# Performance work log

Hardware: AMD Instinct MI355X
Metric: run time of the kernel (lower is better)

The kernel has to match this reference:

```python
import jax, jax.numpy as jnp
import numpy as np

S, IN, M, V, K = 8192, 512, 512, 50, 8


def setup_inputs() -> dict:
    key = jax.random.key(0)
    ks = jax.random.split(key, 6)
    sc = 0.02
    inp = {
        "inputs": jax.random.normal(ks[0], (S, IN), jnp.float32),
        "Wioux": sc * jax.random.normal(ks[1], (5 * M, IN), jnp.float32),
        "bioux": jnp.zeros((5 * M,), jnp.float32),
        "Wiouh": sc * jax.random.normal(ks[2], (5 * M, M), jnp.float32),
        "biouh": jnp.zeros((5 * M,), jnp.float32),
        "Wlx": sc * jax.random.normal(ks[3], (M, IN), jnp.float32),
        "blx": jnp.zeros((M,), jnp.float32),
        "Wlh": sc * jax.random.normal(ks[4], (M, M), jnp.float32),
        "blh": jnp.zeros((M,), jnp.float32),
        "lb": jnp.ones((V, M), jnp.float32),  # nn.Parameter(torch.ones(V, M))
    }
    rng = np.random.default_rng(0)
    t = np.arange(S)[:, None]
    u1 = rng.random((S, K)); u2 = rng.random((S, K))
    rel_fw = (u1 * np.maximum(t, 1)).astype(np.int32)                     # idx < t
    rel_bw = np.minimum(t + 1 + (u2 * np.maximum(S - 1 - t, 1)).astype(np.int64), S - 1).astype(np.int32)  # idx > t
    mask_fw = rng.random((S, K)) < 0.6
    mask_fw[0, :] = False      # t=0 fwd has no relatives in the original
    mask_bw = rng.random((S, K)) < 0.6
    mask_bw[S - 1, :] = False  # t=S-1 bwd has no relatives
    inp["rel_fw"] = jnp.asarray(rel_fw)
    inp["dep_fw"] = jnp.asarray(rng.integers(0, V, (S, K)).astype(np.int32))
    inp["mask_fw"] = jnp.asarray(mask_fw)
    inp["rel_bw"] = jnp.asarray(rel_bw)
    inp["dep_bw"] = jnp.asarray(rng.integers(0, V, (S, K)).astype(np.int32))
    inp["mask_bw"] = jnp.asarray(mask_bw)
    return inp


def _syn_lstm(inputs, Wioux, bioux, Wiouh, biouh, Wlx, blx, Wlh, blh, lb,
              rel, dep, mask, order):
    """One direction; order gives the timestep visit order. Returns [S, M]."""
    mdim = Wlh.shape[0]

    def step(carry, t):
        Hbuf, h_prev, c_prev = carry
        x = inputs[t]
        ious = Wioux @ x + bioux + Wiouh @ h_prev + biouh          # [5M]
        c0, c1, c2, c3, c4 = jnp.split(ious, 5)
        # NOTE: original torch code assigns (i,o,f,s,u)=(sig(i),sig(o),sig(s),sig(f),tanh(u)),
        # i.e. gate f uses chunk 3 and gate s uses chunk 2 -- reproduced faithfully.
        i = jax.nn.sigmoid(c0)
        o = jax.nn.sigmoid(c1)
        f = jax.nn.sigmoid(c3)
        s = jax.nn.sigmoid(c2)
        u = jnp.tanh(c4)
        c = f * c_prev + i * u
        h = o * jnp.tanh(c)
        rel_h = Hbuf[rel[t]]                                       # [K, M] gather of prior hiddens
        l = jax.nn.sigmoid(rel_h @ Wlh.T + blh + (Wlx @ x + blx) + lb[dep[t]])  # [K, M]
        agg = jnp.sum(l * rel_h * mask[t][:, None].astype(rel_h.dtype), axis=0)  # [M]
        h = h + s * jnp.tanh(agg)   # if all masked: agg=0, tanh(0)=0 -> empty-relative branch
        Hbuf = Hbuf.at[t].set(h)
        return (Hbuf, h, c), None

    Hbuf0 = jnp.zeros((inputs.shape[0], mdim), inputs.dtype)
    z = jnp.zeros((mdim,), inputs.dtype)
    (Hbuf, _, _), _ = jax.lax.scan(step, (Hbuf0, z, z), order)
    return Hbuf


def reference(inputs, Wioux, bioux, Wiouh, biouh, Wlx, blx, Wlh, blh, lb,
              rel_fw, dep_fw, mask_fw, rel_bw, dep_bw, mask_bw):
    n = inputs.shape[0]
    Hfw = _syn_lstm(inputs, Wioux, bioux, Wiouh, biouh, Wlx, blx, Wlh, blh, lb,
                    rel_fw, dep_fw, mask_fw, jnp.arange(n))
    Hbw = _syn_lstm(inputs, Wioux, bioux, Wiouh, biouh, Wlx, blx, Wlh, blh, lb,
                    rel_bw, dep_bw, mask_bw, jnp.arange(n - 1, -1, -1))
    return jnp.concatenate([Hfw, Hbw], axis=1)   # [S, 2*M]
```

## Files before the change

kernel.cpp:

```cpp
#include <hip/hip_runtime.h>

#define S_LEN 8192
#define KREL 8
#define WPD 128

typedef float f4 __attribute__((ext_vector_type(4)));
typedef unsigned long long u64;

__device__ __forceinline__ float sigmf(float x) { return 1.0f / (1.0f + __expf(-x)); }
__device__ __forceinline__ float tanhfast(float x) { return 1.0f - 2.0f / (__expf(2.0f * x) + 1.0f); }

__global__ void k_maskcvt(const unsigned char* __restrict__ src,
                          unsigned char* __restrict__ dst, int n)
{
  const unsigned int* w = (const unsigned int*)src;
  __shared__ int s_i32, s_f32;
  if (threadIdx.x == 0) { s_i32 = 1; s_f32 = 1; }
  __syncthreads();
  int i32ok = 1, f32ok = 1;
  for (int i = threadIdx.x; i < 1024; i += blockDim.x) {
    const unsigned int v = w[i];
    if (v != 0u && v != 1u) i32ok = 0;
    if (v != 0u && v != 0x3F800000u) f32ok = 0;
  }
  if (!i32ok) atomicAnd(&s_i32, 0);
  if (!f32ok) atomicAnd(&s_f32, 0);
  __syncthreads();
  const int wide = (s_i32 || s_f32);
  for (int i = blockIdx.x * blockDim.x + threadIdx.x; i < n; i += gridDim.x * blockDim.x)
    dst[i] = wide ? (w[i] ? 1 : 0) : (src[i] ? 1 : 0);
}

__global__ __launch_bounds__(256)
void k_gemm(const float* __restrict__ X, const float* __restrict__ Wioux,
            const float* __restrict__ Wlx, const float* __restrict__ bioux,
            const float* __restrict__ biouh, const float* __restrict__ blx,
            const float* __restrict__ blh, float* __restrict__ P)
{
  __shared__ float As[16][64];
  __shared__ float Bs[16][64];
  const int t0 = blockIdx.x * 64;
  const int r0 = blockIdx.y * 64;
  const int tid = threadIdx.x;
  const int tx = tid & 15, ty = tid >> 4;
  const int si = tid >> 2, sk = (tid & 3) << 2;
  const int rB = r0 + si;
  const float* brow = (rB < 2560) ? (Wioux + (size_t)rB * 512)
                                  : (Wlx + (size_t)(rB - 2560) * 512);
  const float* arow = X + (size_t)(t0 + si) * 512;
  float acc[4][4] = {};
  for (int k0 = 0; k0 < 512; k0 += 16) {
    const float4 av = *(const float4*)(arow + k0 + sk);
    const float4 bv = *(const float4*)(brow + k0 + sk);
    __syncthreads();
    As[sk + 0][si] = av.x; As[sk + 1][si] = av.y; As[sk + 2][si] = av.z; As[sk + 3][si] = av.w;
    Bs[sk + 0][si] = bv.x; Bs[sk + 1][si] = bv.y; Bs[sk + 2][si] = bv.z; Bs[sk + 3][si] = bv.w;
    __syncthreads();
#pragma unroll
    for (int kk = 0; kk < 16; ++kk) {
      const float4 a = *(const float4*)&As[kk][ty * 4];
      const float4 b = *(const float4*)&Bs[kk][tx * 4];
      acc[0][0] += a.x * b.x; acc[0][1] += a.x * b.y; acc[0][2] += a.x * b.z; acc[0][3] += a.x * b.w;
      acc[1][0] += a.y * b.x; acc[1][1] += a.y * b.y; acc[1][2] += a.y * b.z; acc[1][3] += a.y * b.w;
      acc[2][0] += a.z * b.x; acc[2][1] += a.z * b.y; acc[2][2] += a.z * b.z; acc[2][3] += a.z * b.w;
      acc[3][0] += a.w * b.x; acc[3][1] += a.w * b.y; acc[3][2] += a.w * b.z; acc[3][3] += a.w * b.w;
    }
  }
#pragma unroll
  for (int i = 0; i < 4; ++i) {
    const int t = t0 + ty * 4 + i;
#pragma unroll
    for (int j = 0; j < 4; ++j) {
      const int r = r0 + tx * 4 + j;
      const float bias = (r < 2560) ? (bioux[r] + biouh[r]) : (blx[r - 2560] + blh[r - 2560]);
      P[(size_t)t * 3072 + r] = acc[i][j] + bias;
    }
  }
}

__global__ __launch_bounds__(256, 1)
void k_rec(const float* __restrict__ Wiouh, const float* __restrict__ Wlh,
           const float* __restrict__ P, const float* __restrict__ lb,
           const int* __restrict__ rel_fw, const int* __restrict__ dep_fw,
           const unsigned char* __restrict__ mask_fw,
           const int* __restrict__ rel_bw, const int* __restrict__ dep_bw,
           const unsigned char* __restrict__ mask_bw,
           float* __restrict__ Gfw, float* __restrict__ Gbw,
           u64* rec, float* __restrict__ out)
{
  __shared__ float wlds[4 * 6 * 512];
  __shared__ float hs[2][512];
  const int wg  = blockIdx.x;
  const int dir = wg / WPD;
  const int w   = wg % WPD;
  const int tid = threadIdx.x;
  const int grp = tid >> 6;
  const int lane = tid & 63;
  const int kl = lane & 7;
  const int m = w * 4 + grp;
  const int dircol = dir * 512;
  const int* rel = dir ? rel_bw : rel_fw;
  const int* dep = dir ? dep_bw : dep_fw;
  const unsigned char* msk = dir ? mask_bw : mask_fw;
  float* Gbuf = dir ? Gbw : Gfw;

  {
    const float* rows[6];
#pragma unroll
    for (int rg = 0; rg < 5; ++rg) rows[rg] = Wiouh + (size_t)(rg * 512 + m) * 512;
    rows[5] = Wlh + (size_t)m * 512;
#pragma unroll
    for (int rg = 0; rg < 6; ++rg)
#pragma unroll
      for (int q = 0; q < 2; ++q)
        *(f4*)&wlds[(size_t)grp * 3072 + rg * 512 + q * 256 + lane * 4] =
            *(const f4*)(rows[rg] + q * 256 + lane * 4);
  }
  const unsigned wbase = (unsigned)(uintptr_t)&wlds[(size_t)grp * 3072 + lane * 4];

  hs[0][tid] = 0.0f; hs[0][tid + 256] = 0.0f;

  float cstate = 0.0f, hprev = 0.0f, gprev = 0.0f;

  int jjU, mkU, jjN, mkN, depN;
  float Hg, Gg, LBg;
  float p0, p1, p2, p3, p4, p5;
  {
    const int t0 = dir ? (S_LEN - 1) : 0;
    const int t1 = dir ? (S_LEN - 2) : 1;
    jjU = rel[t0 * KREL + kl]; mkU = (int)msk[t0 * KREL + kl];
    Hg  = out[(size_t)jjU * 1024 + dircol + m];
    Gg  = Gbuf[(size_t)jjU * 512 + m];
    LBg = lb[(size_t)dep[t0 * KREL + kl] * 512 + m];
    const float* prow = P + (size_t)t0 * 3072;
    p0 = prow[m];        p1 = prow[512 + m];  p2 = prow[1024 + m];
    p3 = prow[1536 + m]; p4 = prow[2048 + m]; p5 = prow[2560 + m];
    jjN = rel[t1 * KREL + kl]; mkN = (int)msk[t1 * KREL + kl]; depN = dep[t1 * KREL + kl];
  }
  __syncthreads();

#pragma unroll 1
  for (int s = 0; s < S_LEN; ++s) {
    const int t = dir ? (S_LEN - 1 - s) : s;
    const int tn = dir ? (t - 1) : (t + 1);
    const int prevt  = dir ? (t + 1) : (t - 1);
    const int prevt2 = dir ? (t + 2) : (t - 2);

    f4 wf[6][2];
#pragma unroll
    for (int rg = 0; rg < 6; ++rg)
#pragma unroll
      for (int q = 0; q < 2; ++q)
        asm volatile("ds_read_b128 %0, %1 offset:%2"
                     : "=v"(wf[rg][q])
                     : "v"(wbase), "i"((rg * 512 + q * 256) * 4)
                     : "memory");

    if (s > 0) {
      const int pb = (((s - 1) & 1) * 2 + dir) * 512;
      u64 v0 = __hip_atomic_load(rec + pb + tid,       __ATOMIC_RELAXED, __HIP_MEMORY_SCOPE_AGENT);
      u64 v1 = __hip_atomic_load(rec + pb + tid + 256, __ATOMIC_RELAXED, __HIP_MEMORY_SCOPE_AGENT);
      for (;;) {
        const bool ok0 = (unsigned)(v0 >> 32) >= (unsigned)s;
        const bool ok1 = (unsigned)(v1 >> 32) >= (unsigned)s;
        if (ok0 && ok1) break;
        if (!ok0) v0 = __hip_atomic_load(rec + pb + tid,       __ATOMIC_RELAXED, __HIP_MEMORY_SCOPE_AGENT);
        if (!ok1) v1 = __hip_atomic_load(rec + pb + tid + 256, __ATOMIC_RELAXED, __HIP_MEMORY_SCOPE_AGENT);
      }
      hs[s & 1][tid]       = __uint_as_float((unsigned)v0);
      hs[s & 1][tid + 256] = __uint_as_float((unsigned)v1);
      __syncthreads();
    }

    asm volatile("s_waitcnt lgkmcnt(0)" ::: "memory");
    float4 h4[2];
#pragma unroll
    for (int q = 0; q < 2; ++q) h4[q] = *(const float4*)&hs[s & 1][lane * 4 + 256 * q];
    float dsum[6];
#pragma unroll
    for (int rg = 0; rg < 6; ++rg) {
      float a = 0.0f;
#pragma unroll
      for (int q = 0; q < 2; ++q) {
        a += wf[rg][q].x * h4[q].x;
        a += wf[rg][q].y * h4[q].y;
        a += wf[rg][q].z * h4[q].z;
        a += wf[rg][q].w * h4[q].w;
      }
      a += __shfl_xor(a, 1);  a += __shfl_xor(a, 2);  a += __shfl_xor(a, 4);
      a += __shfl_xor(a, 8);  a += __shfl_xor(a, 16); a += __shfl_xor(a, 32);
      dsum[rg] = a;
    }
    const float g = dsum[5];

    const float iv = sigmf(p0 + dsum[0]);
    const float ov = sigmf(p1 + dsum[1]);
    const float sv = sigmf(p2 + dsum[2]);
    const float fv = sigmf(p3 + dsum[3]);
    const float uv = tanhfast(p4 + dsum[4]);
    cstate = fv * cstate + iv * uv;
    const float hb = ov * tanhfast(cstate);

    const float hv_k = (jjU == prevt) ? hprev : Hg;
    const float gv_k = (jjU == prevt) ? g : ((jjU == prevt2) ? gprev : Gg);
    float sm = mkU ? (sigmf(gv_k + p5 + LBg) * hv_k) : 0.0f;
    sm += __shfl_xor(sm, 1); sm += __shfl_xor(sm, 2); sm += __shfl_xor(sm, 4);
    const float hval = hb + sv * tanhfast(sm);

    if (lane == 0) {
      const u64 pk =
          ((u64)(unsigned)(s + 1) << 32) | (u64)__float_as_uint(hval);
      __hip_atomic_store(rec + ((s & 1) * 2 + dir) * 512 + m, pk,
                         __ATOMIC_RELAXED, __HIP_MEMORY_SCOPE_AGENT);
      out[(size_t)t * 1024 + dircol + m] = hval;
      if (s > 0) Gbuf[(size_t)prevt * 512 + m] = g;
    }

    if (s < S_LEN - 1) {
      const float HgN  = out[(size_t)jjN * 1024 + dircol + m];
      const float GgN  = Gbuf[(size_t)jjN * 512 + m];
      const float LBgN = lb[(size_t)depN * 512 + m];
      const float* prow = P + (size_t)tn * 3072;
      p0 = prow[m];        p1 = prow[512 + m];  p2 = prow[1024 + m];
      p3 = prow[1536 + m]; p4 = prow[2048 + m]; p5 = prow[2560 + m];
      int jj2 = jjN, mk2 = mkN, dep2 = depN;
      if (s < S_LEN - 2) {
        const int t2 = dir ? (t - 2) : (t + 2);
        jj2 = rel[t2 * KREL + kl]; mk2 = (int)msk[t2 * KREL + kl]; dep2 = dep[t2 * KREL + kl];
      }
      jjU = jjN; mkU = mkN; Hg = HgN; Gg = GgN; LBg = LBgN;
      jjN = jj2; mkN = mk2; depN = dep2;
    }
    hprev = hval; gprev = g;
  }
}

__global__ void k_fill(float* __restrict__ o, int n, float v)
{ const int i = blockIdx.x * 256 + threadIdx.x; if (i < n) o[i] = v; }

extern "C" void kernel_launch(void* const* d_in, const int* in_sizes, int n_in,
                              void* d_out, int out_size, void* d_ws, size_t ws_size,
                              hipStream_t stream)
{
  (void)in_sizes; (void)n_in;
  const float* X     = (const float*)d_in[0];
  const float* Wioux = (const float*)d_in[1];
  const float* bioux = (const float*)d_in[2];
  const float* Wiouh = (const float*)d_in[3];
  const float* biouh = (const float*)d_in[4];
  const float* Wlx   = (const float*)d_in[5];
  const float* blx   = (const float*)d_in[6];
  const float* Wlh   = (const float*)d_in[7];
  const float* blh   = (const float*)d_in[8];
  const float* lb    = (const float*)d_in[9];
  const int* rel_fw  = (const int*)d_in[10];
  const int* dep_fw  = (const int*)d_in[11];
  const unsigned char* mask_fw_raw = (const unsigned char*)d_in[12];
  const int* rel_bw  = (const int*)d_in[13];
  const int* dep_bw  = (const int*)d_in[14];
  const unsigned char* mask_bw_raw = (const unsigned char*)d_in[15];
  float* out = (float*)d_out;

  const int nmask = S_LEN * KREL;
  const size_t needP = (size_t)S_LEN * 3072 * 4;
  const size_t needG = (size_t)S_LEN * 512 * 4;
  const size_t need  = 32768 + needP + 2 * needG + 2 * (size_t)nmask;
  if (ws_size < need) {
    k_fill<<<(out_size + 255) / 256, 256, 0, stream>>>(out, out_size, 12345.0f);
    return;
  }
  char* ws = (char*)d_ws;
  u64*   rec = (u64*)ws;
  float* P   = (float*)(ws + 32768);
  float* Gfw = (float*)(ws + 32768 + needP);
  float* Gbw = Gfw + (size_t)S_LEN * 512;
  unsigned char* Mfw = (unsigned char*)(ws + 32768 + needP + 2 * needG);
  unsigned char* Mbw = Mfw + nmask;

  hipMemsetAsync(rec, 0, 16384, stream);
  k_maskcvt<<<64, 256, 0, stream>>>(mask_fw_raw, Mfw, nmask);
  k_maskcvt<<<64, 256, 0, stream>>>(mask_bw_raw, Mbw, nmask);
  dim3 gg(S_LEN / 64, 3072 / 64);
  k_gemm<<<gg, 256, 0, stream>>>(X, Wioux, Wlx, bioux, biouh, blx, blh, P);
  k_rec<<<2 * WPD, 256, 0, stream>>>(Wiouh, Wlh, P, lb, rel_fw, dep_fw, Mfw,
                                     rel_bw, dep_bw, Mbw, Gfw, Gbw, rec, out);
}
```

Before: 18.69 ms.

## Replace workgroup barrier with tagged LDS flags and pipelined global polling

The per-step __syncthreads after staging the previous hidden state into LDS is replaced by storing tagged 64-bit (step, value) words into LDS. Each wave spins on its own slice until every tag reaches the current step, so waves no longer wait on the whole workgroup. The global poll loop also keeps three loads in flight to hide polling latency. The cost is doubled LDS footprint for h, more LDS traffic, extra spin loads, and reliance on relaxed atomics for ordering.

Measured after the change: 18.17 ms. 2.8% less time.

```diff
diff --git a/kernel.cpp b/kernel.cpp
--- a/kernel.cpp
+++ b/kernel.cpp
@@ -89,7 +89,7 @@
            u64* rec, float* __restrict__ out)
 {
   __shared__ float wlds[4 * 6 * 512];
-  __shared__ float hs[2][512];
+  __shared__ u64 hs64[2][512];
   const int wg  = blockIdx.x;
   const int dir = wg / WPD;
   const int w   = wg % WPD;
@@ -118,7 +118,8 @@
   }
   const unsigned wbase = (unsigned)(uintptr_t)&wlds[(size_t)grp * 3072 + lane * 4];
 
-  hs[0][tid] = 0.0f; hs[0][tid + 256] = 0.0f;
+  hs64[0][tid] = 0ull; hs64[0][tid + 256] = 0ull;
+  hs64[1][tid] = 0ull; hs64[1][tid + 256] = 0ull;
 
   float cstate = 0.0f, hprev = 0.0f, gprev = 0.0f;
 
@@ -158,34 +159,64 @@
 
     if (s > 0) {
       const int pb = (((s - 1) & 1) * 2 + dir) * 512;
-      u64 v0 = __hip_atomic_load(rec + pb + tid,       __ATOMIC_RELAXED, __HIP_MEMORY_SCOPE_AGENT);
-      u64 v1 = __hip_atomic_load(rec + pb + tid + 256, __ATOMIC_RELAXED, __HIP_MEMORY_SCOPE_AGENT);
+      u64* q0 = rec + pb + tid;
+      u64* q1 = rec + pb + tid + 256;
+      u64 a0 = __hip_atomic_load(q0, __ATOMIC_RELAXED, __HIP_MEMORY_SCOPE_AGENT);
+      u64 a1 = __hip_atomic_load(q1, __ATOMIC_RELAXED, __HIP_MEMORY_SCOPE_AGENT);
+      u64 b0 = __hip_atomic_load(q0, __ATOMIC_RELAXED, __HIP_MEMORY_SCOPE_AGENT);
+      u64 b1 = __hip_atomic_load(q1, __ATOMIC_RELAXED, __HIP_MEMORY_SCOPE_AGENT);
+      u64 c0 = __hip_atomic_load(q0, __ATOMIC_RELAXED, __HIP_MEMORY_SCOPE_AGENT);
+      u64 c1 = __hip_atomic_load(q1, __ATOMIC_RELAXED, __HIP_MEMORY_SCOPE_AGENT);
       for (;;) {
-        const bool ok0 = (unsigned)(v0 >> 32) >= (unsigned)s;
-        const bool ok1 = (unsigned)(v1 >> 32) >= (unsigned)s;
-        if (ok0 && ok1) break;
-        if (!ok0) v0 = __hip_atomic_load(rec + pb + tid,       __ATOMIC_RELAXED, __HIP_MEMORY_SCOPE_AGENT);
-        if (!ok1) v1 = __hip_atomic_load(rec + pb + tid + 256, __ATOMIC_RELAXED, __HIP_MEMORY_SCOPE_AGENT);
+        const bool k0 = (unsigned)(a0 >> 32) >= (unsigned)s;
+        const bool k1 = (unsigned)(a1 >> 32) >= (unsigned)s;
+        if (k0 && k1) break;
+        const u64 n0 = __hip_atomic_load(q0, __ATOMIC_RELAXED, __HIP_MEMORY_SCOPE_AGENT);
+        const u64 n1 = __hip_atomic_load(q1, __ATOMIC_RELAXED, __HIP_MEMORY_SCOPE_AGENT);
+        a0 = k0 ? a0 : b0;  b0 = k0 ? b0 : c0;  c0 = n0;
+        a1 = k1 ? a1 : b1;  b1 = k1 ? b1 : c1;  c1 = n1;
       }
-      hs[s & 1][tid]       = __uint_as_float((unsigned)v0);
-      hs[s & 1][tid + 256] = __uint_as_float((unsigned)v1);
-      __syncthreads();
+      __hip_atomic_store(&hs64[s & 1][tid], a0,
+                         __ATOMIC_RELAXED, __HIP_MEMORY_SCOPE_WORKGROUP);
+      __hip_atomic_store(&hs64[s & 1][tid + 256], a1,
+                         __ATOMIC_RELAXED, __HIP_MEMORY_SCOPE_WORKGROUP);
+    }
+
+    u64 pk0[4], pk1[4];
+    {
+      const int base = lane * 4;
+      for (;;) {
+        unsigned mn = 0xffffffffu;
+#pragma unroll
+        for (int j = 0; j < 4; ++j) {
+          pk0[j] = __hip_atomic_load(&hs64[s & 1][base + j],
+                                     __ATOMIC_RELAXED, __HIP_MEMORY_SCOPE_WORKGROUP);
+          pk1[j] = __hip_atomic_load(&hs64[s & 1][256 + base + j],
+                                     __ATOMIC_RELAXED, __HIP_MEMORY_SCOPE_WORKGROUP);
+          const unsigned t0 = (unsigned)(pk0[j] >> 32);
+          const unsigned t1 = (unsigned)(pk1[j] >> 32);
+          mn = mn < t0 ? mn : t0;
+          mn = mn < t1 ? mn : t1;
+        }
+        if (mn >= (unsigned)s) break;
+      }
     }
 
     asm volatile("s_waitcnt lgkmcnt(0)" ::: "memory");
-    float4 h4[2];
-#pragma unroll
-    for (int q = 0; q < 2; ++q) h4[q] = *(const float4*)&hs[s & 1][lane * 4 + 256 * q];
+    float hx[2][4];
+#pragma unroll
+    for (int j = 0; j < 4; ++j) {
+      hx[0][j] = __uint_as_float((unsigned)pk0[j]);
+      hx[1][j] = __uint_as_float((unsigned)pk1[j]);
+    }
     float dsum[6];
 #pragma unroll
     for (int rg = 0; rg < 6; ++rg) {
       float a = 0.0f;
 #pragma unroll
-      for (int q = 0; q < 2; ++q) {
-        a += wf[rg][q].x * h4[q].x;
-        a += wf[rg][q].y * h4[q].y;
-        a += wf[rg][q].z * h4[q].z;
-        a += wf[rg][q].w * h4[q].w;
+      for (int j = 0; j < 4; ++j) {
+        a += wf[rg][0][j] * hx[0][j];
+        a += wf[rg][1][j] * hx[1][j];
       }
       a += __shfl_xor(a, 1);  a += __shfl_xor(a, 2);  a += __shfl_xor(a, 4);
       a += __shfl_xor(a, 8);  a += __shfl_xor(a, 16); a += __shfl_xor(a, 32);
```

## Replace workgroup barrier with LDS progress flags and pipeline spin loads

Applied to the files above, without the earlier changes.

Replaces the __syncthreads after publishing the received hidden state with per-wave progress counters in LDS that each wave spins on. The global spin loop now keeps three loads in flight per slot to cut polling latency. The relative-aggregation term for non-immediate relatives is computed before the wait, so only the case where the relative is the previous step stays on the critical path. Spinning on LDS flags adds ordering risk and uses more ALU slots while waiting.

Measured after the change: 20.19 ms. 1.08x slower.

```diff
diff --git a/kernel.cpp b/kernel.cpp
--- a/kernel.cpp
+++ b/kernel.cpp
@@ -90,6 +90,7 @@
 {
   __shared__ float wlds[4 * 6 * 512];
   __shared__ float hs[2][512];
+  __shared__ unsigned int wprog[4];
   const int wg  = blockIdx.x;
   const int dir = wg / WPD;
   const int w   = wg % WPD;
@@ -119,6 +120,8 @@
   const unsigned wbase = (unsigned)(uintptr_t)&wlds[(size_t)grp * 3072 + lane * 4];
 
   hs[0][tid] = 0.0f; hs[0][tid + 256] = 0.0f;
+  hs[1][tid] = 0.0f; hs[1][tid + 256] = 0.0f;
+  if (tid < 4) wprog[tid] = 0u;
 
   float cstate = 0.0f, hprev = 0.0f, gprev = 0.0f;
 
@@ -156,26 +159,54 @@
                      : "v"(wbase), "i"((rg * 512 + q * 256) * 4)
                      : "memory");
 
+    const float gv_base = (jjU == prevt2) ? gprev : Gg;
+    const float sm_pre  = mkU ? (sigmf(gv_base + p5 + LBg) * Hg) : 0.0f;
+
     if (s > 0) {
       const int pb = (((s - 1) & 1) * 2 + dir) * 512;
-      u64 v0 = __hip_atomic_load(rec + pb + tid,       __ATOMIC_RELAXED, __HIP_MEMORY_SCOPE_AGENT);
-      u64 v1 = __hip_atomic_load(rec + pb + tid + 256, __ATOMIC_RELAXED, __HIP_MEMORY_SCOPE_AGENT);
+      u64* q0 = rec + pb + tid;
+      u64* q1 = rec + pb + tid + 256;
+      u64 a0 = __hip_atomic_load(q0, __ATOMIC_RELAXED, __HIP_MEMORY_SCOPE_AGENT);
+      u64 a1 = __hip_atomic_load(q1, __ATOMIC_RELAXED, __HIP_MEMORY_SCOPE_AGENT);
+      u64 b0 = __hip_atomic_load(q0, __ATOMIC_RELAXED, __HIP_MEMORY_SCOPE_AGENT);
+      u64 b1 = __hip_atomic_load(q1, __ATOMIC_RELAXED, __HIP_MEMORY_SCOPE_AGENT);
+      u64 c0 = __hip_atomic_load(q0, __ATOMIC_RELAXED, __HIP_MEMORY_SCOPE_AGENT);
+      u64 c1 = __hip_atomic_load(q1, __ATOMIC_RELAXED, __HIP_MEMORY_SCOPE_AGENT);
       for (;;) {
-        const bool ok0 = (unsigned)(v0 >> 32) >= (unsigned)s;
-        const bool ok1 = (unsigned)(v1 >> 32) >= (unsigned)s;
-        if (ok0 && ok1) break;
-        if (!ok0) v0 = __hip_atomic_load(rec + pb + tid,       __ATOMIC_RELAXED, __HIP_MEMORY_SCOPE_AGENT);
-        if (!ok1) v1 = __hip_atomic_load(rec + pb + tid + 256, __ATOMIC_RELAXED, __HIP_MEMORY_SCOPE_AGENT);
+        const bool k0 = (unsigned)(a0 >> 32) >= (unsigned)s;
+        const bool k1 = (unsigned)(a1 >> 32) >= (unsigned)s;
+        if (k0 && k1) break;
+        const u64 n0 = __hip_atomic_load(q0, __ATOMIC_RELAXED, __HIP_MEMORY_SCOPE_AGENT);
+        const u64 n1 = __hip_atomic_load(q1, __ATOMIC_RELAXED, __HIP_MEMORY_SCOPE_AGENT);
+        a0 = k0 ? a0 : b0;  b0 = k0 ? b0 : c0;  c0 = n0;
+        a1 = k1 ? a1 : b1;  b1 = k1 ? b1 : c1;  c1 = n1;
       }
-      hs[s & 1][tid]       = __uint_as_float((unsigned)v0);
-      hs[s & 1][tid + 256] = __uint_as_float((unsigned)v1);
-      __syncthreads();
-    }
-
+      hs[s & 1][tid]       = __uint_as_float((unsigned)a0);
+      hs[s & 1][tid + 256] = __uint_as_float((unsigned)a1);
+      asm volatile("s_waitcnt lgkmcnt(0)" ::: "memory");
+      if (lane == 0)
+        __hip_atomic_store(&wprog[grp], (unsigned)s,
+                           __ATOMIC_RELAXED, __HIP_MEMORY_SCOPE_WORKGROUP);
+    }
+
+    if (s > 0) {
+      for (;;) {
+        const unsigned w0 = __hip_atomic_load(&wprog[0], __ATOMIC_RELAXED, __HIP_MEMORY_SCOPE_WORKGROUP);
+        const unsigned w1 = __hip_atomic_load(&wprog[1], __ATOMIC_RELAXED, __HIP_MEMORY_SCOPE_WORKGROUP);
+        const unsigned w2 = __hip_atomic_load(&wprog[2], __ATOMIC_RELAXED, __HIP_MEMORY_SCOPE_WORKGROUP);
+        const unsigned w3 = __hip_atomic_load(&wprog[3], __ATOMIC_RELAXED, __HIP_MEMORY_SCOPE_WORKGROUP);
+        unsigned mn = w0 < w1 ? w0 : w1;
+        mn = mn < w2 ? mn : w2;
+        mn = mn < w3 ? mn : w3;
+        if (mn >= (unsigned)s) break;
+      }
+      asm volatile("" ::: "memory");
+    }
+
+    float4 h4[2];
+    h4[0] = *(const float4*)&hs[s & 1][lane * 4];
+    h4[1] = *(const float4*)&hs[s & 1][256 + lane * 4];
     asm volatile("s_waitcnt lgkmcnt(0)" ::: "memory");
-    float4 h4[2];
-#pragma unroll
-    for (int q = 0; q < 2; ++q) h4[q] = *(const float4*)&hs[s & 1][lane * 4 + 256 * q];
     float dsum[6];
 #pragma unroll
     for (int rg = 0; rg < 6; ++rg) {
@@ -201,9 +232,8 @@
     cstate = fv * cstate + iv * uv;
     const float hb = ov * tanhfast(cstate);
 
-    const float hv_k = (jjU == prevt) ? hprev : Hg;
-    const float gv_k = (jjU == prevt) ? g : ((jjU == prevt2) ? gprev : Gg);
-    float sm = mkU ? (sigmf(gv_k + p5 + LBg) * hv_k) : 0.0f;
+    const float smf = mkU ? (sigmf(g + p5 + LBg) * hprev) : 0.0f;
+    float sm = (jjU == prevt) ? smf : sm_pre;
     sm += __shfl_xor(sm, 1); sm += __shfl_xor(sm, 2); sm += __shfl_xor(sm, 4);
     const float hval = hb + sv * tanhfast(sm);
 
```
